# Kernel tuning notes

Measured on AMD Instinct MI355X. Metric: run time of the kernel, lower is better.

The kernel has to match this reference:

```python
import jax, jax.numpy as jnp
import numpy as np

W_BIT = 8

def quantize_weight(w, k=W_BIT):
    # DoReFa-style weight quantization (conv2d_Q_fn): tanh-normalize to [0,1],
    # uniform-quantize to 2^k-1 levels (round with straight-through), map to [-1,1].
    n = float(2 ** k - 1)
    t = jnp.tanh(w)
    t = t / (2.0 * jnp.max(jnp.abs(t))) + 0.5
    q = t + jax.lax.stop_gradient(jnp.round(t * n) / n - t)
    return 2.0 * q - 1.0

def qconv(x, w, b, pad):
    wq = quantize_weight(w)
    y = jax.lax.conv_general_dilated(
        x, wq, window_strides=(1, 1), padding=[(pad, pad), (pad, pad)],
        dimension_numbers=('NCHW', 'OIHW', 'NCHW'))
    return y + b[None, :, None, None]

def upsample2x(x):
    # nearest-neighbor, scale_factor=2
    return jnp.repeat(jnp.repeat(x, 2, axis=2), 2, axis=3)

def setup_inputs() -> dict:
    key = jax.random.key(0)
    ks = jax.random.split(key, 11)
    F = 256
    C3 = jax.random.normal(ks[0], (8, 512, 64, 64), dtype=jnp.float32)
    C4 = jax.random.normal(ks[1], (8, 1024, 32, 32), dtype=jnp.float32)
    C5 = jax.random.normal(ks[2], (8, 2048, 16, 16), dtype=jnp.float32)
    # conv params (torch nn.Conv2d default has bias)
    w5 = jax.random.normal(ks[3], (F, 2048, 1, 1), dtype=jnp.float32) * 0.02
    b5 = jax.random.normal(ks[4], (F,), dtype=jnp.float32) * 0.01
    w4 = jax.random.normal(ks[5], (F, 1024, 1, 1), dtype=jnp.float32) * 0.02
    b4 = jax.random.normal(ks[6], (F,), dtype=jnp.float32) * 0.01
    w3 = jax.random.normal(ks[7], (F, 512, 1, 1), dtype=jnp.float32) * 0.02
    b3 = jax.random.normal(ks[8], (F,), dtype=jnp.float32) * 0.01
    w3_2 = jax.random.normal(ks[9], (F, F, 3, 3), dtype=jnp.float32) * 0.02
    b3_2 = jax.random.normal(ks[10], (F,), dtype=jnp.float32) * 0.01
    return {"C3": C3, "C4": C4, "C5": C5,
            "w5": w5, "b5": b5, "w4": w4, "b4": b4,
            "w3": w3, "b3": b3, "w3_2": w3_2, "b3_2": b3_2}

def reference(C3, C4, C5, w5, b5, w4, b4, w3, b3, w3_2, b3_2):
    P5_x = qconv(C5, w5, b5, pad=0)            # [B,256,16,16]
    P5_up = upsample2x(P5_x)                   # [B,256,32,32]
    P4_x = qconv(C4, w4, b4, pad=0) + P5_up    # [B,256,32,32]
    P4_up = upsample2x(P4_x)                   # [B,256,64,64]
    P3_x = qconv(C3, w3, b3, pad=0) + P4_up    # [B,256,64,64]
    P3_x = qconv(P3_x, w3_2, b3_2, pad=1)      # [B,256,64,64]
    return P3_x
```

## Files before the change

### kernel.cpp

```cpp
#include <hip/hip_runtime.h>
#include <stdint.h>

typedef unsigned short u16;
typedef short s16x8 __attribute__((ext_vector_type(8)));
typedef short s16x4 __attribute__((ext_vector_type(4)));
typedef float f32x4 __attribute__((ext_vector_type(4)));
typedef unsigned int u32x4 __attribute__((ext_vector_type(4)));

__device__ __forceinline__ u16 f2bf(float x) {
    unsigned u = __float_as_uint(x);
    unsigned r = u + 0x7FFFu + ((u >> 16) & 1u);
    return (u16)(r >> 16);
}
__device__ __forceinline__ float bf2f(u16 h) {
    return __uint_as_float((unsigned)h << 16);
}

__device__ __forceinline__ void gll16(void* lds, const void* g) {
    __builtin_amdgcn_global_load_lds(
        (const __attribute__((address_space(1))) void*)g,
        (__attribute__((address_space(3))) void*)lds,
        16, 0, 0);
}

__global__ __launch_bounds__(256) void reduce_maxabs(
    const float* __restrict__ a0, int n0, const float* __restrict__ a1, int n1,
    const float* __restrict__ a2, int n2, const float* __restrict__ a3, int n3,
    float* __restrict__ out) {
    int which = blockIdx.y;
    const float* w = which == 0 ? a0 : which == 1 ? a1 : which == 2 ? a2 : a3;
    int n = which == 0 ? n0 : which == 1 ? n1 : which == 2 ? n2 : n3;
    float m = 0.f;
    for (int i = blockIdx.x * 256 + threadIdx.x; i < n; i += gridDim.x * 256)
        m = fmaxf(m, fabsf(w[i]));
#pragma unroll
    for (int off = 32; off > 0; off >>= 1)
        m = fmaxf(m, __shfl_down(m, off, 64));
    __shared__ float sm[4];
    if ((threadIdx.x & 63) == 0) sm[threadIdx.x >> 6] = m;
    __syncthreads();
    if (threadIdx.x == 0) {
        m = fmaxf(fmaxf(sm[0], sm[1]), fmaxf(sm[2], sm[3]));
        atomicMax((int*)out + which, __float_as_int(m));
    }
}

__global__ __launch_bounds__(256) void quant_w(
    const float* __restrict__ w5, const float* __restrict__ w4,
    const float* __restrict__ w3, const float* __restrict__ w32,
    const float* __restrict__ mx,
    u16* __restrict__ q5, u16* __restrict__ q4,
    u16* __restrict__ q3, u16* __restrict__ q2) {
    int b = blockIdx.x, t = threadIdx.x;
    int which, i;
    const float* w;
    if (b < 2048)      { which = 0; w = w5;  i = b * 256 + t; }
    else if (b < 3072) { which = 1; w = w4;  i = (b - 2048) * 256 + t; }
    else if (b < 3584) { which = 2; w = w3;  i = (b - 3072) * 256 + t; }
    else               { which = 3; w = w32; i = (b - 3584) * 256 + t; }
    float inv = 0.5f / tanhf(mx[which]);
    float tt = tanhf(w[i]) * inv + 0.5f;
    float q = rintf(tt * 255.f) * (1.f / 255.f);
    u16 o = f2bf(2.f * q - 1.f);
    if (which == 0) q5[i] = o;
    else if (which == 1) q4[i] = o;
    else if (which == 2) q3[i] = o;
    else {
        int kw = i % 3, kh = (i / 3) % 3, c = (i / 9) & 255, f = i / 2304;
        q2[(size_t)((kh * 3 + kw) * 256 + f) * 256 + c] = o;
    }
}

__global__ __launch_bounds__(256) void transpose_nhwc(
    const float* __restrict__ C5, const float* __restrict__ C4,
    const float* __restrict__ C3,
    u16* __restrict__ c5n, u16* __restrict__ c4n, u16* __restrict__ c3n) {
    __shared__ float tile[128][65];
    int t = threadIdx.x, b = blockIdx.x;
    const float* src; u16* dst; int C, HW, cb, hwb, nn;
    if (b < 512)       { nn = b >> 6; int r = b & 63; cb = r >> 2; hwb = r & 3;
                         C = 2048; HW = 256;  src = C5; dst = c5n; }
    else if (b < 1536) { int l = b - 512;  nn = l >> 7; int r = l & 127; cb = r >> 4; hwb = r & 15;
                         C = 1024; HW = 1024; src = C4; dst = c4n; }
    else               { int l = b - 1536; nn = l >> 8; int r = l & 255; cb = r >> 6; hwb = r & 63;
                         C = 512;  HW = 4096; src = C3; dst = c3n; }
    int c0 = cb << 7, hw0 = hwb << 6;
    const float* s2 = src + (size_t)nn * C * HW;
#pragma unroll
    for (int i = 0; i < 8; ++i) {
        int c = (t >> 4) + (i << 4);
        int hw = (t & 15) << 2;
        f32x4 v = *(const f32x4*)(s2 + (size_t)(c0 + c) * HW + hw0 + hw);
        tile[c][hw] = v.x; tile[c][hw + 1] = v.y; tile[c][hw + 2] = v.z; tile[c][hw + 3] = v.w;
    }
    __syncthreads();
    u16* d2 = dst + (size_t)nn * C * HW;
    int g = t & 15;
#pragma unroll
    for (int i = 0; i < 4; ++i) {
        int hw = (t >> 4) + (i << 4);
        s16x8 o;
#pragma unroll
        for (int jj = 0; jj < 8; ++jj) {
            int j = (jj + g) & 7;
            o[j] = (short)f2bf(tile[8 * g + j][hw]);
        }
        *(s16x8*)(d2 + (size_t)(hw0 + hw) * C + c0 + 8 * g) = o;
    }
}

template<int BF, int BPX, int FJ, int FI>
__global__ __launch_bounds__(256) void gemm_qconv(
    const u16* __restrict__ A, const u16* __restrict__ B,
    const float* __restrict__ bias,
    const float* __restrict__ addF, const float* __restrict__ addF2,
    const u16* __restrict__ addB,
    float* __restrict__ outF, u16* __restrict__ outB,
    int Kfull, int Kchunk, int Wlog, int HWlog, size_t zstride) {
    __shared__ u16 As[BF * 64];
    __shared__ u16 Bs[BPX * 64];
    int t = threadIdx.x, lane = t & 63, wv = t >> 6;
    int l16 = lane & 15, quad = lane >> 4;
    int f0 = blockIdx.y * BF, p0 = blockIdx.x * BPX;
    int wf = (wv >> 1) * (BF / 2), wp = (wv & 1) * (BPX / 2);
    f32x4 acc[FJ][FI] = {};
    const u16* Ab = A + (size_t)f0 * Kfull;
    const u16* Bb = B + (size_t)p0 * Kfull;
    int row = t >> 3, c8 = t & 7;
    int k_begin = blockIdx.z * Kchunk, k_end = k_begin + Kchunk;
    for (int k0 = k_begin; k0 < k_end; k0 += 64) {
#pragma unroll
        for (int it = 0; it < BF / 32; ++it)
            gll16(&As[(it * 256 + wv * 64) * 8], Ab + (size_t)(it * 32 + row) * Kfull + k0 + c8 * 8);
#pragma unroll
        for (int it = 0; it < BPX / 32; ++it)
            gll16(&Bs[(it * 256 + wv * 64) * 8], Bb + (size_t)(it * 32 + row) * Kfull + k0 + c8 * 8);
        __syncthreads();
#pragma unroll
        for (int kk = 0; kk < 64; kk += 32) {
            s16x8 a[FJ], b[FI];
#pragma unroll
            for (int j = 0; j < FJ; ++j)
                a[j] = *(const s16x8*)&As[(wf + 16 * j + l16) * 64 + kk + quad * 8];
#pragma unroll
            for (int i = 0; i < FI; ++i)
                b[i] = *(const s16x8*)&Bs[(wp + 16 * i + l16) * 64 + kk + quad * 8];
#pragma unroll
            for (int j = 0; j < FJ; ++j)
#pragma unroll
                for (int i = 0; i < FI; ++i)
                    acc[j][i] = __builtin_amdgcn_mfma_f32_16x16x32_bf16(a[j], b[i], acc[j][i], 0, 0, 0);
        }
        __syncthreads();
    }
    int W = 1 << Wlog;
    bool bias_on = (blockIdx.z == 0);
    float* outFz = outF ? outF + blockIdx.z * zstride : outF;
#pragma unroll
    for (int j = 0; j < FJ; ++j) {
        int f = f0 + wf + 16 * j + (quad << 2);
        f32x4 bz = {0.f, 0.f, 0.f, 0.f};
        if (bias_on && bias) bz = *(const f32x4*)(bias + f);
#pragma unroll
        for (int i = 0; i < FI; ++i) {
            int px = p0 + wp + 16 * i + l16;
            f32x4 v = acc[j][i] + bz;
            if (addF || addB) {
                int nn = px >> HWlog;
                int rem = px & ((1 << HWlog) - 1);
                int h = rem >> Wlog, ww = rem & (W - 1);
                int sp = (nn << (HWlog - 2)) + ((h >> 1) << (Wlog - 1)) + (ww >> 1);
                if (addF) {
                    f32x4 s = *(const f32x4*)(addF + (size_t)sp * 256 + f);
                    if (addF2) s += *(const f32x4*)(addF2 + (size_t)sp * 256 + f);
                    v += s;
                } else {
                    s16x4 av = *(const s16x4*)(addB + (size_t)sp * 256 + f);
                    v.x += bf2f((u16)av.x); v.y += bf2f((u16)av.y);
                    v.z += bf2f((u16)av.z); v.w += bf2f((u16)av.w);
                }
            }
            if (outB) {
                s16x4 o;
                o.x = (short)f2bf(v.x); o.y = (short)f2bf(v.y);
                o.z = (short)f2bf(v.z); o.w = (short)f2bf(v.w);
                *(s16x4*)(outB + (size_t)px * 256 + f) = o;
            } else {
                *(f32x4*)(outFz + (size_t)px * 256 + f) = v;
            }
        }
    }
}

#define CVS 40
__global__ __launch_bounds__(256) void conv3x3_q(
    const u16* __restrict__ X, const u16* __restrict__ Wq,
    const float* __restrict__ bias, float* __restrict__ outp) {
    __shared__ u16 Rg[6 * 66 * CVS];
    __shared__ u16 Aw[5 * 64 * CVS];
    int t = threadIdx.x, lane = t & 63, wv = t >> 6;
    int l16 = lane & 15, quad = lane >> 4;
    int n = blockIdx.x >> 4, h0 = (blockIdx.x & 15) << 2;
    int f0 = blockIdx.y << 6;
    f32x4 acc[4][4] = {};
    for (int c0 = 0; c0 < 256; c0 += 32) {
#pragma unroll
        for (int it = 0; it < 7; ++it) {
            int chunk = it * 256 + t;
            if (chunk < 1584) {
                int r = chunk / 264;
                int rest = chunk - r * 264;
                int w = rest >> 2, c8 = rest & 3;
                int h = h0 - 1 + r, ww = w - 1;
                u32x4 v; v.x = 0; v.y = 0; v.z = 0; v.w = 0;
                if ((unsigned)h < 64u && (unsigned)ww < 64u)
                    v = *(const u32x4*)(X + ((((size_t)n << 12) + (h << 6) + ww) << 8) + c0 + c8 * 8);
                *(u32x4*)(Rg + (r * 66 + w) * CVS + c8 * 8) = v;
            }
        }
#pragma unroll
        for (int it = 0; it < 5; ++it) {
            int chunk = it * 256 + t;
            int tap = chunk >> 8, fr = (chunk >> 2) & 63, cc = chunk & 3;
            *(u32x4*)(Aw + (tap * 64 + fr) * CVS + cc * 8) =
                *(const u32x4*)(Wq + (((size_t)tap * 256 + f0 + fr) << 8) + c0 + cc * 8);
        }
        __syncthreads();
#pragma unroll
        for (int tp = 0; tp < 5; ++tp) {
            int dh = tp / 3, dw = tp % 3;
            s16x8 a[4], b[4];
#pragma unroll
            for (int i = 0; i < 4; ++i)
                b[i] = *(const s16x8*)(Rg + ((wv + dh) * 66 + 16 * i + l16 + dw) * CVS + quad * 8);
#pragma unroll
            for (int j = 0; j < 4; ++j)
                a[j] = *(const s16x8*)(Aw + (tp * 64 + 16 * j + l16) * CVS + quad * 8);
#pragma unroll
            for (int j = 0; j < 4; ++j)
#pragma unroll
                for (int i = 0; i < 4; ++i)
                    acc[j][i] = __builtin_amdgcn_mfma_f32_16x16x32_bf16(a[j], b[i], acc[j][i], 0, 0, 0);
        }
        __syncthreads();
#pragma unroll
        for (int it = 0; it < 4; ++it) {
            int chunk = it * 256 + t;
            int tap = 5 + (chunk >> 8), fr = (chunk >> 2) & 63, cc = chunk & 3;
            *(u32x4*)(Aw + ((tap - 5) * 64 + fr) * CVS + cc * 8) =
                *(const u32x4*)(Wq + (((size_t)tap * 256 + f0 + fr) << 8) + c0 + cc * 8);
        }
        __syncthreads();
#pragma unroll
        for (int tp = 5; tp < 9; ++tp) {
            int dh = tp / 3, dw = tp % 3;
            s16x8 a[4], b[4];
#pragma unroll
            for (int i = 0; i < 4; ++i)
                b[i] = *(const s16x8*)(Rg + ((wv + dh) * 66 + 16 * i + l16 + dw) * CVS + quad * 8);
#pragma unroll
            for (int j = 0; j < 4; ++j)
                a[j] = *(const s16x8*)(Aw + ((tp - 5) * 64 + 16 * j + l16) * CVS + quad * 8);
#pragma unroll
            for (int j = 0; j < 4; ++j)
#pragma unroll
                for (int i = 0; i < 4; ++i)
                    acc[j][i] = __builtin_amdgcn_mfma_f32_16x16x32_bf16(a[j], b[i], acc[j][i], 0, 0, 0);
        }
        __syncthreads();
    }
    int h = h0 + wv;
#pragma unroll
    for (int j = 0; j < 4; ++j) {
        int f = f0 + 16 * j + (quad << 2);
        f32x4 bz = *(const f32x4*)(bias + f);
#pragma unroll
        for (int i = 0; i < 4; ++i) {
            int w = 16 * i + l16;
#pragma unroll
            for (int r = 0; r < 4; ++r)
                outp[((size_t)(n * 256 + f + r) << 12) + (h << 6) + w] = acc[j][i][r] + bz[r];
        }
    }
}

extern "C" void kernel_launch(void* const* d_in, const int* in_sizes, int n_in,
                              void* d_out, int out_size, void* d_ws, size_t ws_size,
                              hipStream_t stream) {
    (void)in_sizes; (void)n_in; (void)out_size; (void)ws_size;
    const float* C3  = (const float*)d_in[0];
    const float* C4  = (const float*)d_in[1];
    const float* C5  = (const float*)d_in[2];
    const float* w5  = (const float*)d_in[3];
    const float* b5  = (const float*)d_in[4];
    const float* w4  = (const float*)d_in[5];
    const float* b4  = (const float*)d_in[6];
    const float* w3  = (const float*)d_in[7];
    const float* b3  = (const float*)d_in[8];
    const float* w32 = (const float*)d_in[9];
    const float* b32 = (const float*)d_in[10];
    float* outp = (float*)d_out;

    char* p = (char*)d_ws;
    float* mx = (float*)p;  p += 256;
    u16* q5   = (u16*)p;    p += (size_t)524288 * 2;
    u16* q4   = (u16*)p;    p += (size_t)262144 * 2;
    u16* q3   = (u16*)p;    p += (size_t)131072 * 2;
    u16* q2   = (u16*)p;    p += (size_t)589824 * 2;
    u16* c5n  = (u16*)p;    p += (size_t)4194304 * 2;
    u16* c4n  = (u16*)p;    p += (size_t)8388608 * 2;
    u16* c3n  = (u16*)p;    p += (size_t)16777216 * 2;
    float* p5xa = (float*)p; p += (size_t)2097152 * 4;
    float* p5xb = (float*)p; p += (size_t)2097152 * 4;
    u16* p4x  = (u16*)p;    p += (size_t)8388608 * 2;
    u16* p3xn = (u16*)p;    p += (size_t)8388608 * 2;

    hipMemsetAsync(mx, 0, 256, stream);
    reduce_maxabs<<<dim3(128, 4), 256, 0, stream>>>(w5, 524288, w4, 262144,
                                                    w3, 131072, w32, 589824, mx);
    quant_w<<<5888, 256, 0, stream>>>(w5, w4, w3, w32, mx, q5, q4, q3, q2);
    transpose_nhwc<<<3584, 256, 0, stream>>>(C5, C4, C3, c5n, c4n, c3n);
    gemm_qconv<64, 64, 2, 2><<<dim3(32, 4, 2), 256, 0, stream>>>(
        q5, c5n, b5, nullptr, nullptr, nullptr, p5xa, nullptr,
        2048, 1024, 4, 8, (size_t)2097152);
    gemm_qconv<64, 128, 2, 4><<<dim3(64, 4, 1), 256, 0, stream>>>(
        q4, c4n, b4, p5xa, p5xb, nullptr, nullptr, p4x,
        1024, 1024, 5, 10, 0);
    gemm_qconv<128, 128, 4, 4><<<dim3(256, 2, 1), 256, 0, stream>>>(
        q3, c3n, b3, nullptr, nullptr, p4x, nullptr, p3xn,
        512, 512, 6, 12, 0);
    conv3x3_q<<<dim3(128, 4), 256, 0, stream>>>(p3xn, q2, b32, outp);
}
```

Measured before the change: 292.5 us.

## Shrink transpose tile to bf16 64x64 and stage conv3x3 weights per row

The NCHW-to-NHWC transpose now converts to bf16 before writing LDS, using a 64x64 bf16 tile instead of a 128x64 fp32 tile and launching twice as many blocks. Channel pairs are packed into 32-bit LDS writes, and reads are 16-byte vector loads. Separately, the 3x3 conv stages weights three taps at a time (one kernel row), shrinking the weight LDS buffer from 5 to 3 taps. Both changes reduce LDS footprint to raise occupancy, at the cost of an extra barrier per channel chunk in the conv.

```diff
diff --git a/kernel.cpp b/kernel.cpp
--- a/kernel.cpp
+++ b/kernel.cpp
@@ -75,37 +75,39 @@
     const float* __restrict__ C5, const float* __restrict__ C4,
     const float* __restrict__ C3,
     u16* __restrict__ c5n, u16* __restrict__ c4n, u16* __restrict__ c3n) {
-    __shared__ float tile[128][65];
+    __shared__ u16 tl[64 * 66];
     int t = threadIdx.x, b = blockIdx.x;
     const float* src; u16* dst; int C, HW, cb, hwb, nn;
-    if (b < 512)       { nn = b >> 6; int r = b & 63; cb = r >> 2; hwb = r & 3;
+    if (b < 1024)      { nn = b >> 7; int r = b & 127; cb = r >> 2; hwb = r & 3;
                          C = 2048; HW = 256;  src = C5; dst = c5n; }
-    else if (b < 1536) { int l = b - 512;  nn = l >> 7; int r = l & 127; cb = r >> 4; hwb = r & 15;
+    else if (b < 3072) { int l = b - 1024; nn = l >> 8; int r = l & 255; cb = r >> 4; hwb = r & 15;
                          C = 1024; HW = 1024; src = C4; dst = c4n; }
-    else               { int l = b - 1536; nn = l >> 8; int r = l & 255; cb = r >> 6; hwb = r & 63;
+    else               { int l = b - 3072; nn = l >> 9; int r = l & 511; cb = r >> 6; hwb = r & 63;
                          C = 512;  HW = 4096; src = C3; dst = c3n; }
-    int c0 = cb << 7, hw0 = hwb << 6;
+    int c0 = cb << 6, hw0 = hwb << 6;
     const float* s2 = src + (size_t)nn * C * HW;
-#pragma unroll
-    for (int i = 0; i < 8; ++i) {
-        int c = (t >> 4) + (i << 4);
-        int hw = (t & 15) << 2;
-        f32x4 v = *(const f32x4*)(s2 + (size_t)(c0 + c) * HW + hw0 + hw);
-        tile[c][hw] = v.x; tile[c][hw + 1] = v.y; tile[c][hw + 2] = v.z; tile[c][hw + 3] = v.w;
+    int q = t & 15, rr = t >> 4;
+    int hwl = q << 2;
+#pragma unroll
+    for (int i = 0; i < 2; ++i) {
+        int cp = 2 * rr + 32 * i;
+        f32x4 v0 = *(const f32x4*)(s2 + (size_t)(c0 + cp) * HW + hw0 + hwl);
+        f32x4 v1 = *(const f32x4*)(s2 + (size_t)(c0 + cp + 1) * HW + hw0 + hwl);
+#pragma unroll
+        for (int k = 0; k < 4; ++k) {
+            unsigned pk = (unsigned)f2bf(v0[k]) | ((unsigned)f2bf(v1[k]) << 16);
+            *(unsigned*)&tl[(hwl + k) * 66 + cp] = pk;
+        }
     }
     __syncthreads();
     u16* d2 = dst + (size_t)nn * C * HW;
-    int g = t & 15;
-#pragma unroll
-    for (int i = 0; i < 4; ++i) {
-        int hw = (t >> 4) + (i << 4);
-        s16x8 o;
-#pragma unroll
-        for (int jj = 0; jj < 8; ++jj) {
-            int j = (jj + g) & 7;
-            o[j] = (short)f2bf(tile[8 * g + j][hw]);
-        }
-        *(s16x8*)(d2 + (size_t)(hw0 + hw) * C + c0 + 8 * g) = o;
+#pragma unroll
+    for (int i = 0; i < 2; ++i) {
+        int chunk = t + 256 * i;
+        int hw = chunk >> 3, g = chunk & 7;
+        const unsigned* pr = (const unsigned*)&tl[hw * 66 + 8 * g];
+        u32x4 o; o.x = pr[0]; o.y = pr[1]; o.z = pr[2]; o.w = pr[3];
+        *(u32x4*)(d2 + (size_t)(hw0 + hw) * C + c0 + 8 * g) = o;
     }
 }
 
@@ -197,7 +199,7 @@
     const u16* __restrict__ X, const u16* __restrict__ Wq,
     const float* __restrict__ bias, float* __restrict__ outp) {
     __shared__ u16 Rg[6 * 66 * CVS];
-    __shared__ u16 Aw[5 * 64 * CVS];
+    __shared__ u16 Aw[3 * 64 * CVS];
     int t = threadIdx.x, lane = t & 63, wv = t >> 6;
     int l16 = lane & 15, quad = lane >> 4;
     int n = blockIdx.x >> 4, h0 = (blockIdx.x & 15) << 2;
@@ -219,55 +221,33 @@
             }
         }
 #pragma unroll
-        for (int it = 0; it < 5; ++it) {
-            int chunk = it * 256 + t;
-            int tap = chunk >> 8, fr = (chunk >> 2) & 63, cc = chunk & 3;
-            *(u32x4*)(Aw + (tap * 64 + fr) * CVS + cc * 8) =
-                *(const u32x4*)(Wq + (((size_t)tap * 256 + f0 + fr) << 8) + c0 + cc * 8);
-        }
-        __syncthreads();
-#pragma unroll
-        for (int tp = 0; tp < 5; ++tp) {
-            int dh = tp / 3, dw = tp % 3;
-            s16x8 a[4], b[4];
-#pragma unroll
-            for (int i = 0; i < 4; ++i)
-                b[i] = *(const s16x8*)(Rg + ((wv + dh) * 66 + 16 * i + l16 + dw) * CVS + quad * 8);
-#pragma unroll
-            for (int j = 0; j < 4; ++j)
-                a[j] = *(const s16x8*)(Aw + (tp * 64 + 16 * j + l16) * CVS + quad * 8);
-#pragma unroll
-            for (int j = 0; j < 4; ++j)
+        for (int grp = 0; grp < 3; ++grp) {
+#pragma unroll
+            for (int it = 0; it < 3; ++it) {
+                int chunk = it * 256 + t;
+                int tl = chunk >> 8, fr = (chunk >> 2) & 63, cc = chunk & 3;
+                *(u32x4*)(Aw + (tl * 64 + fr) * CVS + cc * 8) =
+                    *(const u32x4*)(Wq + (((size_t)(3 * grp + tl) * 256 + f0 + fr) << 8) + c0 + cc * 8);
+            }
+            __syncthreads();
+            int dh = grp;
+#pragma unroll
+            for (int dw = 0; dw < 3; ++dw) {
+                s16x8 a[4], b[4];
 #pragma unroll
                 for (int i = 0; i < 4; ++i)
-                    acc[j][i] = __builtin_amdgcn_mfma_f32_16x16x32_bf16(a[j], b[i], acc[j][i], 0, 0, 0);
-        }
-        __syncthreads();
-#pragma unroll
-        for (int it = 0; it < 4; ++it) {
-            int chunk = it * 256 + t;
-            int tap = 5 + (chunk >> 8), fr = (chunk >> 2) & 63, cc = chunk & 3;
-            *(u32x4*)(Aw + ((tap - 5) * 64 + fr) * CVS + cc * 8) =
-                *(const u32x4*)(Wq + (((size_t)tap * 256 + f0 + fr) << 8) + c0 + cc * 8);
-        }
-        __syncthreads();
-#pragma unroll
-        for (int tp = 5; tp < 9; ++tp) {
-            int dh = tp / 3, dw = tp % 3;
-            s16x8 a[4], b[4];
-#pragma unroll
-            for (int i = 0; i < 4; ++i)
-                b[i] = *(const s16x8*)(Rg + ((wv + dh) * 66 + 16 * i + l16 + dw) * CVS + quad * 8);
-#pragma unroll
-            for (int j = 0; j < 4; ++j)
-                a[j] = *(const s16x8*)(Aw + ((tp - 5) * 64 + 16 * j + l16) * CVS + quad * 8);
-#pragma unroll
-            for (int j = 0; j < 4; ++j)
-#pragma unroll
-                for (int i = 0; i < 4; ++i)
-                    acc[j][i] = __builtin_amdgcn_mfma_f32_16x16x32_bf16(a[j], b[i], acc[j][i], 0, 0, 0);
-        }
-        __syncthreads();
+                    b[i] = *(const s16x8*)(Rg + ((wv + dh) * 66 + 16 * i + l16 + dw) * CVS + quad * 8);
+#pragma unroll
+                for (int j = 0; j < 4; ++j)
+                    a[j] = *(const s16x8*)(Aw + (dw * 64 + 16 * j + l16) * CVS + quad * 8);
+#pragma unroll
+                for (int j = 0; j < 4; ++j)
+#pragma unroll
+                    for (int i = 0; i < 4; ++i)
+                        acc[j][i] = __builtin_amdgcn_mfma_f32_16x16x32_bf16(a[j], b[i], acc[j][i], 0, 0, 0);
+            }
+            __syncthreads();
+        }
     }
     int h = h0 + wv;
 #pragma unroll
@@ -319,7 +299,7 @@
     reduce_maxabs<<<dim3(128, 4), 256, 0, stream>>>(w5, 524288, w4, 262144,
                                                     w3, 131072, w32, 589824, mx);
     quant_w<<<5888, 256, 0, stream>>>(w5, w4, w3, w32, mx, q5, q4, q3, q2);
-    transpose_nhwc<<<3584, 256, 0, stream>>>(C5, C4, C3, c5n, c4n, c3n);
+    transpose_nhwc<<<7168, 256, 0, stream>>>(C5, C4, C3, c5n, c4n, c3n);
     gemm_qconv<64, 64, 2, 2><<<dim3(32, 4, 2), 256, 0, stream>>>(
         q5, c5n, b5, nullptr, nullptr, nullptr, p5xa, nullptr,
         2048, 1024, 4, 8, (size_t)2097152);
```

Result: no change. 296.5 us (+1.4%).
